# Optimization experiments

Hardware: AMD Instinct MI355X
Metric: run time of the kernel (lower is better)

The kernel has to match this reference:

```python
import jax, jax.numpy as jnp
import numpy as np

D_THRE = 0.03  # spatial-consistency distance threshold from forward call
N_POINTS = 32768


def _pairwise_dist(x):
    """x: [M, 3] -> [M, M] Euclidean distance matrix, safe-sqrt (zero diag)."""
    diff = x[:, None, :] - x[None, :, :]          # [M, M, 3]
    sq = jnp.sum(diff * diff, axis=-1)            # [M, M]
    safe = jnp.where(sq > 0, sq, 1.0)
    return jnp.where(sq > 0, jnp.sqrt(safe), 0.0)


def setup_inputs() -> dict:
    key = jax.random.key(0)
    k1, k2 = jax.random.split(key)
    num_clusters = 64
    cluster_size = N_POINTS // num_clusters
    # LiDAR-scale point cloud (meters)
    pc1 = jax.random.normal(k1, (1, N_POINTS, 3), dtype=jnp.float32) * 20.0
    flow = jax.random.normal(k2, (1, N_POINTS, 3), dtype=jnp.float32) * 0.1
    # DBSCAN labels are constants computed at __init__; model them as
    # contiguous equal-size clusters so the ragged loop is jit-friendly.
    labels = jnp.arange(N_POINTS, dtype=jnp.int32) // cluster_size
    return {"flow": flow, "pc1": pc1, "labels": labels, "num_clusters": num_clusters}


def reference(flow, pc1, labels, num_clusters):
    n = pc1.shape[1]
    m = n // num_clusters  # points per cluster (labels are contiguous blocks)
    pc1_deformed = pc1 + flow
    src = pc1[0].reshape(num_clusters, m, 3)           # cluster gather == reshape
    tgt = pc1_deformed[0].reshape(num_clusters, m, 3)

    def cluster_sc_loss(s, t):
        # spatial_consistency_loss (SC2-PCR measure) for one cluster
        src_dist = _pairwise_dist(s)                   # [M, M]
        tgt_dist = _pairwise_dist(t)                   # [M, M]
        cross = jnp.abs(src_dist - tgt_dist)
        sc_measure = jnp.clip(1.0 - (cross * cross) / (D_THRE * D_THRE), 0.0)
        return jnp.mean(1.0 - sc_measure)

    losses = jax.vmap(cluster_sc_loss)(src, tgt)       # [K]
    loss_sc = jnp.sum(losses) / num_clusters
    return loss_sc
```

## Files before the change

kernel.cpp:

```cpp
#include <hip/hip_runtime.h>

#define M 512
#define K 64
#define TP 64
#define NT 256
#define QPB 4
#define NQ  9

__device__ __constant__ unsigned char TA_tab[36] = {
    0,0,0,0,0,0,0,0, 1,1,1,1,1,1,1, 2,2,2,2,2,2, 3,3,3,3,3, 4,4,4,4, 5,5,5, 6,6, 7};
__device__ __constant__ unsigned char TB_tab[36] = {
    0,1,2,3,4,5,6,7, 1,2,3,4,5,6,7, 2,3,4,5,6,7, 3,4,5,6,7, 4,5,6,7, 5,6,7, 6,7, 7};

__global__ __launch_bounds__(NT) void sc_fused_kernel(
    const float* __restrict__ flow,
    const float* __restrict__ pc1,
    float* __restrict__ out)
{
    __shared__ __align__(16) float P[M][8];
    __shared__ float wsum[NT / 64];

    const int c   = blockIdx.x / NQ;
    const int q   = blockIdx.x - c * NQ;
    const int tid = threadIdx.x;
    const int base = c * (M * 3);

    const float inv_d = 1.0f / 0.03f;

#pragma unroll
    for (int i = 0; i < (M * 3) / NT; ++i) {
        const int idx = tid + i * NT;
        const float p = pc1[base + idx];
        const float f = flow[base + idx];
        const int pt   = idx / 3;
        const int comp = idx - pt * 3;
        P[pt][comp]     = p * inv_d;
        P[pt][comp + 4] = (p + f) * inv_d;
    }
    __syncthreads();

    const int lane = tid & 63;
    const int wave = tid >> 6;

    float acc = 0.0f;

#pragma unroll
    for (int t = 0; t < QPB; ++t) {
        const int p = q * QPB + t;
        const int a = TA_tab[p];
        const int b = TB_tab[p];

        const float4 cs = *(const float4*)&P[b * TP + lane][0];
        const float4 ct = *(const float4*)&P[b * TP + lane][4];

        float tacc = 0.0f;
        const int r0 = a * TP + wave * (TP / 4);
#pragma unroll
        for (int rr = 0; rr < TP / 4; ++rr) {
            const float4 rs = *(const float4*)&P[r0 + rr][0];
            const float4 rt = *(const float4*)&P[r0 + rr][4];

            const float dx = rs.x - cs.x, dy = rs.y - cs.y, dz = rs.z - cs.z;
            const float ds = __builtin_amdgcn_sqrtf(dx * dx + dy * dy + dz * dz);
            const float ex = rt.x - ct.x, ey = rt.y - ct.y, ez = rt.z - ct.z;
            const float dt = __builtin_amdgcn_sqrtf(ex * ex + ey * ey + ez * ez);
            const float m = fminf(fabsf(ds - dt), 1.0f);
            tacc = fmaf(m, m, tacc);
        }
        acc += (a == b) ? tacc : (tacc + tacc);
    }

    for (int off = 32; off > 0; off >>= 1)
        acc += __shfl_down(acc, off, 64);
    if (lane == 0) wsum[wave] = acc;
    __syncthreads();
    if (tid == 0) {
        const float s = wsum[0] + wsum[1] + wsum[2] + wsum[3];
        atomicAdd(out, s * (1.0f / 16777216.0f));
    }
}

extern "C" void kernel_launch(void* const* d_in, const int* in_sizes, int n_in,
                              void* d_out, int out_size, void* d_ws, size_t ws_size,
                              hipStream_t stream)
{
    const float* flow = (const float*)d_in[0];
    const float* pc1  = (const float*)d_in[1];
    float* out = (float*)d_out;

    sc_fused_kernel<<<K * NQ, NT, 0, stream>>>(flow, pc1, out);
}
```

Measured before the change: 71.33 us.

## Split work into one block per tile and add a separate reduction kernel

Each block now handles a single 64x64 tile pair instead of four, launching 2304 blocks instead of 576. Each block loads only the two 64-point slices it needs rather than the whole 512-point cluster. The atomicAdd to the output is replaced by per-block partials in the workspace, summed by a second single-block kernel. The goal is more parallelism and less redundant staging per block, at the cost of an extra kernel launch and more block scheduling overhead.

```diff
diff --git a/kernel.cpp b/kernel.cpp
--- a/kernel.cpp
+++ b/kernel.cpp
@@ -4,80 +4,94 @@
 #define K 64
 #define TP 64
 #define NT 256
-#define QPB 4
-#define NQ  9
+#define NTILES 36
 
 __device__ __constant__ unsigned char TA_tab[36] = {
     0,0,0,0,0,0,0,0, 1,1,1,1,1,1,1, 2,2,2,2,2,2, 3,3,3,3,3, 4,4,4,4, 5,5,5, 6,6, 7};
 __device__ __constant__ unsigned char TB_tab[36] = {
     0,1,2,3,4,5,6,7, 1,2,3,4,5,6,7, 2,3,4,5,6,7, 3,4,5,6,7, 4,5,6,7, 5,6,7, 6,7, 7};
 
-__global__ __launch_bounds__(NT) void sc_fused_kernel(
+__global__ __launch_bounds__(NT) void sc_tile_kernel(
     const float* __restrict__ flow,
     const float* __restrict__ pc1,
-    float* __restrict__ out)
+    float* __restrict__ part)
 {
-    __shared__ __align__(16) float P[M][8];
+    __shared__ __align__(16) float Pl[2 * TP][8];
     __shared__ float wsum[NT / 64];
 
-    const int c   = blockIdx.x / NQ;
-    const int q   = blockIdx.x - c * NQ;
+    const int blk = blockIdx.x;
+    const int c   = blk / NTILES;
+    const int p   = blk - c * NTILES;
+    const int a   = TA_tab[p];
+    const int b   = TB_tab[p];
     const int tid = threadIdx.x;
+
+    const float inv_d = 1.0f / 0.03f;
     const int base = c * (M * 3);
 
-    const float inv_d = 1.0f / 0.03f;
-
 #pragma unroll
-    for (int i = 0; i < (M * 3) / NT; ++i) {
-        const int idx = tid + i * NT;
-        const float p = pc1[base + idx];
-        const float f = flow[base + idx];
-        const int pt   = idx / 3;
-        const int comp = idx - pt * 3;
-        P[pt][comp]     = p * inv_d;
-        P[pt][comp + 4] = (p + f) * inv_d;
+    for (int it = 0; it < 2; ++it) {
+        const int idx = tid + it * NT;
+        if (idx < 6 * TP) {
+            const int pt   = idx / 3;
+            const int comp = idx - pt * 3;
+            const int spt  = (pt < TP) ? (a * TP + pt) : (b * TP + (pt - TP));
+            const int g    = base + spt * 3 + comp;
+            const float pv = pc1[g];
+            const float fv = flow[g];
+            Pl[pt][comp]     = pv * inv_d;
+            Pl[pt][comp + 4] = (pv + fv) * inv_d;
+        }
     }
     __syncthreads();
 
     const int lane = tid & 63;
     const int wave = tid >> 6;
 
+    const float4 cs = *(const float4*)&Pl[TP + lane][0];
+    const float4 ct = *(const float4*)&Pl[TP + lane][4];
+
     float acc = 0.0f;
+    const int r0 = wave * (TP / 4);
+#pragma unroll
+    for (int rr = 0; rr < TP / 4; ++rr) {
+        const float4 rs = *(const float4*)&Pl[r0 + rr][0];
+        const float4 rt = *(const float4*)&Pl[r0 + rr][4];
 
-#pragma unroll
-    for (int t = 0; t < QPB; ++t) {
-        const int p = q * QPB + t;
-        const int a = TA_tab[p];
-        const int b = TB_tab[p];
-
-        const float4 cs = *(const float4*)&P[b * TP + lane][0];
-        const float4 ct = *(const float4*)&P[b * TP + lane][4];
-
-        float tacc = 0.0f;
-        const int r0 = a * TP + wave * (TP / 4);
-#pragma unroll
-        for (int rr = 0; rr < TP / 4; ++rr) {
-            const float4 rs = *(const float4*)&P[r0 + rr][0];
-            const float4 rt = *(const float4*)&P[r0 + rr][4];
-
-            const float dx = rs.x - cs.x, dy = rs.y - cs.y, dz = rs.z - cs.z;
-            const float ds = __builtin_amdgcn_sqrtf(dx * dx + dy * dy + dz * dz);
-            const float ex = rt.x - ct.x, ey = rt.y - ct.y, ez = rt.z - ct.z;
-            const float dt = __builtin_amdgcn_sqrtf(ex * ex + ey * ey + ez * ez);
-            const float m = fminf(fabsf(ds - dt), 1.0f);
-            tacc = fmaf(m, m, tacc);
-        }
-        acc += (a == b) ? tacc : (tacc + tacc);
+        const float dx = rs.x - cs.x, dy = rs.y - cs.y, dz = rs.z - cs.z;
+        const float ds = __builtin_amdgcn_sqrtf(dx * dx + dy * dy + dz * dz);
+        const float ex = rt.x - ct.x, ey = rt.y - ct.y, ez = rt.z - ct.z;
+        const float dt = __builtin_amdgcn_sqrtf(ex * ex + ey * ey + ez * ez);
+        const float m = fminf(fabsf(ds - dt), 1.0f);
+        acc = fmaf(m, m, acc);
     }
+    if (a != b) acc += acc;
 
     for (int off = 32; off > 0; off >>= 1)
         acc += __shfl_down(acc, off, 64);
     if (lane == 0) wsum[wave] = acc;
     __syncthreads();
-    if (tid == 0) {
-        const float s = wsum[0] + wsum[1] + wsum[2] + wsum[3];
-        atomicAdd(out, s * (1.0f / 16777216.0f));
-    }
+    if (tid == 0)
+        part[blk] = wsum[0] + wsum[1] + wsum[2] + wsum[3];
+}
+
+__global__ __launch_bounds__(NT) void sc_reduce_kernel(
+    const float* __restrict__ part,
+    float* __restrict__ out)
+{
+    __shared__ float wsum[NT / 64];
+    float s = 0.0f;
+#pragma unroll
+    for (int i = 0; i < (K * NTILES) / NT; ++i)
+        s += part[threadIdx.x + i * NT];
+    for (int off = 32; off > 0; off >>= 1)
+        s += __shfl_down(s, off, 64);
+    const int lane = threadIdx.x & 63;
+    const int wave = threadIdx.x >> 6;
+    if (lane == 0) wsum[wave] = s;
+    __syncthreads();
+    if (threadIdx.x == 0)
+        out[0] = (wsum[0] + wsum[1] + wsum[2] + wsum[3]) * (1.0f / 16777216.0f);
 }
 
 extern "C" void kernel_launch(void* const* d_in, const int* in_sizes, int n_in,
@@ -86,7 +100,9 @@
 {
     const float* flow = (const float*)d_in[0];
     const float* pc1  = (const float*)d_in[1];
-    float* out = (float*)d_out;
+    float* out  = (float*)d_out;
+    float* part = (float*)d_ws;
 
-    sc_fused_kernel<<<K * NQ, NT, 0, stream>>>(flow, pc1, out);
+    sc_tile_kernel<<<K * NTILES, NT, 0, stream>>>(flow, pc1, part);
+    sc_reduce_kernel<<<1, NT, 0, stream>>>(part, out);
 }
```

After: 68.07 us. -4.6%, faster.

## Split work into two tile-pairs per block and stage only needed rows

Applied to the files above, without the earlier changes.

Blocks now each handle two 64x64 tile pairs instead of four, so the grid grows from 576 to 1152 blocks. Each block loads only the row tiles it needs into a small shared buffer, and reads its column points straight from global memory into registers, instead of staging the whole 512-point cluster. This cuts per-block load and shared-memory cost and adds parallelism. In exchange there are more atomics, column data is loaded redundantly across blocks, and each block does less work to amortise launch overhead.

```diff
diff --git a/kernel.cpp b/kernel.cpp
--- a/kernel.cpp
+++ b/kernel.cpp
@@ -4,8 +4,9 @@
 #define K 64
 #define TP 64
 #define NT 256
-#define QPB 4
-#define NQ  9
+#define NPAIRS 36
+#define PPB 2
+#define NBLK (K * NPAIRS / PPB)
 
 __device__ __constant__ unsigned char TA_tab[36] = {
     0,0,0,0,0,0,0,0, 1,1,1,1,1,1,1, 2,2,2,2,2,2, 3,3,3,3,3, 4,4,4,4, 5,5,5, 6,6, 7};
@@ -17,58 +18,66 @@
     const float* __restrict__ pc1,
     float* __restrict__ out)
 {
-    __shared__ __align__(16) float P[M][8];
+    __shared__ __align__(16) float Rows[PPB][TP][8];
     __shared__ float wsum[NT / 64];
 
-    const int c   = blockIdx.x / NQ;
-    const int q   = blockIdx.x - c * NQ;
+    const int blk = blockIdx.x;
+    const int gp0 = blk * PPB;
+    const int c   = gp0 / NPAIRS;
+    const int p0  = gp0 - c * NPAIRS;
     const int tid = threadIdx.x;
+
+    const float inv_d = 1.0f / 0.03f;
     const int base = c * (M * 3);
 
-    const float inv_d = 1.0f / 0.03f;
-
 #pragma unroll
-    for (int i = 0; i < (M * 3) / NT; ++i) {
-        const int idx = tid + i * NT;
-        const float p = pc1[base + idx];
-        const float f = flow[base + idx];
-        const int pt   = idx / 3;
-        const int comp = idx - pt * 3;
-        P[pt][comp]     = p * inv_d;
-        P[pt][comp + 4] = (p + f) * inv_d;
+    for (int it = 0; it < 2; ++it) {
+        const int idx = tid + it * NT;
+        if (idx < PPB * TP * 3) {
+            const int t    = idx / (TP * 3);
+            const int rem  = idx - t * (TP * 3);
+            const int pt   = rem / 3;
+            const int comp = rem - pt * 3;
+            const int a    = TA_tab[p0 + t];
+            const int g    = base + (a * TP + pt) * 3 + comp;
+            const float pv = pc1[g];
+            const float fv = flow[g];
+            Rows[t][pt][comp]     = pv * inv_d;
+            Rows[t][pt][comp + 4] = (pv + fv) * inv_d;
+        }
     }
-    __syncthreads();
 
     const int lane = tid & 63;
     const int wave = tid >> 6;
+    const int t    = wave >> 1;
+    const int half = wave & 1;
+
+    const int a = TA_tab[p0 + t];
+    const int b = TB_tab[p0 + t];
+
+    const int cg = base + (b * TP + lane) * 3;
+    const float px = pc1[cg + 0], py = pc1[cg + 1], pz = pc1[cg + 2];
+    const float fx = flow[cg + 0], fy = flow[cg + 1], fz = flow[cg + 2];
+    const float cs_x = px * inv_d,        cs_y = py * inv_d,        cs_z = pz * inv_d;
+    const float ct_x = (px + fx) * inv_d, ct_y = (py + fy) * inv_d, ct_z = (pz + fz) * inv_d;
+
+    __syncthreads();
 
     float acc = 0.0f;
+    const int r0 = half * (TP / 2);
+#pragma unroll
+    for (int rr = 0; rr < TP / 2; ++rr) {
+        const float4 rs = *(const float4*)&Rows[t][r0 + rr][0];
+        const float4 rt = *(const float4*)&Rows[t][r0 + rr][4];
 
-#pragma unroll
-    for (int t = 0; t < QPB; ++t) {
-        const int p = q * QPB + t;
-        const int a = TA_tab[p];
-        const int b = TB_tab[p];
-
-        const float4 cs = *(const float4*)&P[b * TP + lane][0];
-        const float4 ct = *(const float4*)&P[b * TP + lane][4];
-
-        float tacc = 0.0f;
-        const int r0 = a * TP + wave * (TP / 4);
-#pragma unroll
-        for (int rr = 0; rr < TP / 4; ++rr) {
-            const float4 rs = *(const float4*)&P[r0 + rr][0];
-            const float4 rt = *(const float4*)&P[r0 + rr][4];
-
-            const float dx = rs.x - cs.x, dy = rs.y - cs.y, dz = rs.z - cs.z;
-            const float ds = __builtin_amdgcn_sqrtf(dx * dx + dy * dy + dz * dz);
-            const float ex = rt.x - ct.x, ey = rt.y - ct.y, ez = rt.z - ct.z;
-            const float dt = __builtin_amdgcn_sqrtf(ex * ex + ey * ey + ez * ez);
-            const float m = fminf(fabsf(ds - dt), 1.0f);
-            tacc = fmaf(m, m, tacc);
-        }
-        acc += (a == b) ? tacc : (tacc + tacc);
+        const float dx = rs.x - cs_x, dy = rs.y - cs_y, dz = rs.z - cs_z;
+        const float ds = __builtin_amdgcn_sqrtf(dx * dx + dy * dy + dz * dz);
+        const float ex = rt.x - ct_x, ey = rt.y - ct_y, ez = rt.z - ct_z;
+        const float dt = __builtin_amdgcn_sqrtf(ex * ex + ey * ey + ez * ez);
+        const float m = fminf(fabsf(ds - dt), 1.0f);
+        acc = fmaf(m, m, acc);
     }
+    if (a != b) acc += acc;
 
     for (int off = 32; off > 0; off >>= 1)
         acc += __shfl_down(acc, off, 64);
@@ -88,5 +97,5 @@
     const float* pc1  = (const float*)d_in[1];
     float* out = (float*)d_out;
 
-    sc_fused_kernel<<<K * NQ, NT, 0, stream>>>(flow, pc1, out);
+    sc_fused_kernel<<<NBLK, NT, 0, stream>>>(flow, pc1, out);
 }
```

Result: slower. 76.13 us (+6.7%).
